# Optimization experiments

Hardware: AMD Instinct MI355X
Metric: run time of the kernel (lower is better)

Reference implementation:

```python
import jax, jax.numpy as jnp
import numpy as np


def setup_inputs() -> dict:
    key = jax.random.key(0)
    ks = jax.random.split(key, 8)
    N, E, F, H = 50000, 400000, 128, 512
    x = jax.random.normal(ks[0], (N, F), dtype=jnp.float32)
    edge_index = jax.random.randint(ks[1], (2, E), 0, N, dtype=jnp.int32)
    W1 = jax.random.normal(ks[2], (H, 2 * F), dtype=jnp.float32) * 0.05
    b1 = jax.random.normal(ks[3], (H,), dtype=jnp.float32) * 0.05
    W2 = jax.random.normal(ks[4], (H, 2 * H), dtype=jnp.float32) * 0.05
    b2 = jax.random.normal(ks[5], (H,), dtype=jnp.float32) * 0.05
    Wo = jax.random.normal(ks[6], (1, H), dtype=jnp.float32) * 0.05
    bo = jax.random.normal(ks[7], (1,), dtype=jnp.float32) * 0.05
    return {"x": x, "edge_index": edge_index, "W1": W1, "b1": b1,
            "W2": W2, "b2": b2, "Wo": Wo, "bo": bo}


def reference(x, edge_index, W1, b1, W2, b2, Wo, bo):
    # GraphSAGE mean aggregation: agg[dst] = mean over incoming edges of h[src]
    N = x.shape[0]
    src = edge_index[0]
    dst = edge_index[1]
    deg = jax.ops.segment_sum(jnp.ones_like(dst, dtype=x.dtype), dst,
                              num_segments=N)
    inv_deg = 1.0 / jnp.maximum(deg, 1.0)  # clamp_min(1.0)

    def agg_mean(h):
        s = jax.ops.segment_sum(h[src], dst, num_segments=N)  # [N, D]
        return s * inv_deg[:, None]

    # Layer 1: concat(self, neigh) -> Linear -> ReLU (dropout = identity, eval)
    n1 = agg_mean(x)
    h1 = jax.nn.relu(jnp.concatenate([x, n1], axis=1) @ W1.T + b1)
    # Layer 2
    n2 = agg_mean(h1)
    h2 = jax.nn.relu(jnp.concatenate([h1, n2], axis=1) @ W2.T + b2)
    # Output head
    logits = h2 @ Wo.T + bo  # [N, 1]
    return jax.nn.sigmoid(logits)
```

## Files before the change

### kernel.cpp

```cpp
#include <hip/hip_runtime.h>
#include <math.h>


typedef __attribute__((ext_vector_type(8))) short bf16x8;
typedef __attribute__((ext_vector_type(4))) float f32x4;

static inline int ceil_div(int a, int b) { return (a + b - 1) / b; }

__device__ inline float bf2f_lo(unsigned u) { return __builtin_bit_cast(float, u << 16); }
__device__ inline float bf2f_hi(unsigned u) { return __builtin_bit_cast(float, u & 0xffff0000u); }
__device__ inline unsigned f2bf(float f) {
    unsigned u = __builtin_bit_cast(unsigned, f);
    u += 0x7fffu + ((u >> 16) & 1u);
    return u >> 16;
}

#define GLOAD_LDS16(gp, lp)                                                   \
    __builtin_amdgcn_global_load_lds(                                         \
        (__attribute__((address_space(1))) void*)(gp),                        \
        (__attribute__((address_space(3))) void*)(lp), 16, 0, 0)


__global__ void cvt3_hist_kernel(const float* __restrict__ a, unsigned short* __restrict__ ao, int na4,
                                 const float* __restrict__ b, unsigned short* __restrict__ bo, int nb4,
                                 const float* __restrict__ c, unsigned short* __restrict__ co, int nc4,
                                 const int* __restrict__ dst, int* __restrict__ deg, int E,
                                 int cvt_blocks) {
    if ((int)blockIdx.x < cvt_blocks) {
        int i = blockIdx.x * 256 + threadIdx.x;
        const float* in; unsigned short* out; int k;
        if (i < na4)                  { in = a; out = ao; k = i; }
        else if (i < na4 + nb4)       { in = b; out = bo; k = i - na4; }
        else if (i < na4 + nb4 + nc4) { in = c; out = co; k = i - na4 - nb4; }
        else return;
        float4 v = ((const float4*)in)[k];
        ushort4 o;
        o.x = (unsigned short)f2bf(v.x);
        o.y = (unsigned short)f2bf(v.y);
        o.z = (unsigned short)f2bf(v.z);
        o.w = (unsigned short)f2bf(v.w);
        ((ushort4*)out)[k] = o;
    } else {
        int e = (blockIdx.x - cvt_blocks) * 256 + threadIdx.x;
        if (e < E) atomicAdd(&deg[dst[e]], 1);
    }
}


__global__ __launch_bounds__(256) void chunk_reduce(const int* __restrict__ deg,
                                                    int* __restrict__ partial, int N) {
    int base = blockIdx.x * 1024;
    int s = 0;
    for (int i = threadIdx.x; i < 1024; i += 256) {
        int idx = base + i;
        if (idx < N) s += deg[idx];
    }
    #pragma unroll
    for (int off = 32; off; off >>= 1) s += __shfl_down(s, off);
    __shared__ int ws[4];
    if ((threadIdx.x & 63) == 0) ws[threadIdx.x >> 6] = s;
    __syncthreads();
    if (threadIdx.x == 0) partial[blockIdx.x] = ws[0] + ws[1] + ws[2] + ws[3];
}

__global__ void partial_scan(int* __restrict__ partial, int* __restrict__ rowstartN, int P) {
    int lane = threadIdx.x;
    int v = (lane < P) ? partial[lane] : 0;
    int incl = v;
    #pragma unroll
    for (int off = 1; off < 64; off <<= 1) {
        int t = __shfl_up(incl, off);
        if (lane >= off) incl += t;
    }
    if (lane < P) partial[lane] = incl - v;
    if (lane == 63) *rowstartN = incl;
}

__global__ __launch_bounds__(256) void chunk_scan(const int* __restrict__ deg,
                                                  const int* __restrict__ partial,
                                                  int* __restrict__ rowstart,
                                                  int* __restrict__ cursor, int N) {
    int base = blockIdx.x * 1024 + threadIdx.x * 4;
    int v[4];
    #pragma unroll
    for (int j = 0; j < 4; ++j) {
        int i = base + j;
        v[j] = (i < N) ? deg[i] : 0;
    }
    int mysum = v[0] + v[1] + v[2] + v[3];
    int incl = mysum;
    int lane = threadIdx.x & 63, wave = threadIdx.x >> 6;
    #pragma unroll
    for (int off = 1; off < 64; off <<= 1) {
        int t = __shfl_up(incl, off);
        if (lane >= off) incl += t;
    }
    __shared__ int ws[4];
    if (lane == 63) ws[wave] = incl;
    __syncthreads();
    int run = partial[blockIdx.x] + incl - mysum;
    for (int w = 0; w < wave; ++w) run += ws[w];
    #pragma unroll
    for (int j = 0; j < 4; ++j) {
        int i = base + j;
        if (i < N) { rowstart[i] = run; cursor[i] = run; }
        run += v[j];
    }
}

__global__ void bucket_kernel(const int* __restrict__ src, const int* __restrict__ dst,
                              int* __restrict__ cursor, int* __restrict__ ebuf, int E) {
    int e = blockIdx.x * 256 + threadIdx.x;
    if (e < E) {
        int pos = atomicAdd(&cursor[dst[e]], 1);
        ebuf[pos] = src[e];
    }
}


__global__ void gather_mean_128(const int* __restrict__ rowstart, const int* __restrict__ ebuf,
                                const unsigned* __restrict__ featb, unsigned* __restrict__ outb, int N) {
    int w = (blockIdx.x * blockDim.x + threadIdx.x) >> 6;
    int lane = threadIdx.x & 63;
    if (w >= N) return;
    int e0 = rowstart[w], e1 = rowstart[w + 1];
    float ax = 0.0f, ay = 0.0f;
    int i = e0;
    for (; i + 8 <= e1; i += 8) {
        unsigned v0 = featb[(size_t)ebuf[i]     * 64 + lane];
        unsigned v1 = featb[(size_t)ebuf[i + 1] * 64 + lane];
        unsigned v2 = featb[(size_t)ebuf[i + 2] * 64 + lane];
        unsigned v3 = featb[(size_t)ebuf[i + 3] * 64 + lane];
        unsigned v4 = featb[(size_t)ebuf[i + 4] * 64 + lane];
        unsigned v5 = featb[(size_t)ebuf[i + 5] * 64 + lane];
        unsigned v6 = featb[(size_t)ebuf[i + 6] * 64 + lane];
        unsigned v7 = featb[(size_t)ebuf[i + 7] * 64 + lane];
        ax += bf2f_lo(v0) + bf2f_lo(v1) + bf2f_lo(v2) + bf2f_lo(v3)
            + bf2f_lo(v4) + bf2f_lo(v5) + bf2f_lo(v6) + bf2f_lo(v7);
        ay += bf2f_hi(v0) + bf2f_hi(v1) + bf2f_hi(v2) + bf2f_hi(v3)
            + bf2f_hi(v4) + bf2f_hi(v5) + bf2f_hi(v6) + bf2f_hi(v7);
    }
    for (; i < e1; ++i) {
        unsigned v = featb[(size_t)ebuf[i] * 64 + lane];
        ax += bf2f_lo(v); ay += bf2f_hi(v);
    }
    float inv = 1.0f / fmaxf((float)(e1 - e0), 1.0f);
    outb[(size_t)w * 64 + lane] = f2bf(ax * inv) | (f2bf(ay * inv) << 16);
}

__global__ void gather_mean_512(const int* __restrict__ rowstart, const int* __restrict__ ebuf,
                                const unsigned short* __restrict__ featb,
                                unsigned short* __restrict__ outb, int N) {
    int w = (blockIdx.x * blockDim.x + threadIdx.x) >> 6;
    int lane = threadIdx.x & 63;
    if (w >= N) return;
    int e0 = rowstart[w], e1 = rowstart[w + 1];
    float a[8] = {0, 0, 0, 0, 0, 0, 0, 0};
    const uint4* base = (const uint4*)featb;
    int i = e0;
    for (; i + 8 <= e1; i += 8) {
        uint4 v0 = base[(size_t)ebuf[i]     * 64 + lane];
        uint4 v1 = base[(size_t)ebuf[i + 1] * 64 + lane];
        uint4 v2 = base[(size_t)ebuf[i + 2] * 64 + lane];
        uint4 v3 = base[(size_t)ebuf[i + 3] * 64 + lane];
        uint4 v4 = base[(size_t)ebuf[i + 4] * 64 + lane];
        uint4 v5 = base[(size_t)ebuf[i + 5] * 64 + lane];
        uint4 v6 = base[(size_t)ebuf[i + 6] * 64 + lane];
        uint4 v7 = base[(size_t)ebuf[i + 7] * 64 + lane];
        a[0] += bf2f_lo(v0.x) + bf2f_lo(v1.x) + bf2f_lo(v2.x) + bf2f_lo(v3.x)
              + bf2f_lo(v4.x) + bf2f_lo(v5.x) + bf2f_lo(v6.x) + bf2f_lo(v7.x);
        a[1] += bf2f_hi(v0.x) + bf2f_hi(v1.x) + bf2f_hi(v2.x) + bf2f_hi(v3.x)
              + bf2f_hi(v4.x) + bf2f_hi(v5.x) + bf2f_hi(v6.x) + bf2f_hi(v7.x);
        a[2] += bf2f_lo(v0.y) + bf2f_lo(v1.y) + bf2f_lo(v2.y) + bf2f_lo(v3.y)
              + bf2f_lo(v4.y) + bf2f_lo(v5.y) + bf2f_lo(v6.y) + bf2f_lo(v7.y);
        a[3] += bf2f_hi(v0.y) + bf2f_hi(v1.y) + bf2f_hi(v2.y) + bf2f_hi(v3.y)
              + bf2f_hi(v4.y) + bf2f_hi(v5.y) + bf2f_hi(v6.y) + bf2f_hi(v7.y);
        a[4] += bf2f_lo(v0.z) + bf2f_lo(v1.z) + bf2f_lo(v2.z) + bf2f_lo(v3.z)
              + bf2f_lo(v4.z) + bf2f_lo(v5.z) + bf2f_lo(v6.z) + bf2f_lo(v7.z);
        a[5] += bf2f_hi(v0.z) + bf2f_hi(v1.z) + bf2f_hi(v2.z) + bf2f_hi(v3.z)
              + bf2f_hi(v4.z) + bf2f_hi(v5.z) + bf2f_hi(v6.z) + bf2f_hi(v7.z);
        a[6] += bf2f_lo(v0.w) + bf2f_lo(v1.w) + bf2f_lo(v2.w) + bf2f_lo(v3.w)
              + bf2f_lo(v4.w) + bf2f_lo(v5.w) + bf2f_lo(v6.w) + bf2f_lo(v7.w);
        a[7] += bf2f_hi(v0.w) + bf2f_hi(v1.w) + bf2f_hi(v2.w) + bf2f_hi(v3.w)
              + bf2f_hi(v4.w) + bf2f_hi(v5.w) + bf2f_hi(v6.w) + bf2f_hi(v7.w);
    }
    for (; i < e1; ++i) {
        uint4 v = base[(size_t)ebuf[i] * 64 + lane];
        a[0] += bf2f_lo(v.x); a[1] += bf2f_hi(v.x);
        a[2] += bf2f_lo(v.y); a[3] += bf2f_hi(v.y);
        a[4] += bf2f_lo(v.z); a[5] += bf2f_hi(v.z);
        a[6] += bf2f_lo(v.w); a[7] += bf2f_hi(v.w);
    }
    float inv = 1.0f / fmaxf((float)(e1 - e0), 1.0f);
    uint4 o;
    o.x = f2bf(a[0] * inv) | (f2bf(a[1] * inv) << 16);
    o.y = f2bf(a[2] * inv) | (f2bf(a[3] * inv) << 16);
    o.z = f2bf(a[4] * inv) | (f2bf(a[5] * inv) << 16);
    o.w = f2bf(a[6] * inv) | (f2bf(a[7] * inv) << 16);
    ((uint4*)outb)[(size_t)w * 64 + lane] = o;
}

__global__ __launch_bounds__(256) void gemm_mfma(
    const unsigned short* __restrict__ A0,
    const unsigned short* __restrict__ A1,
    const unsigned short* __restrict__ W,
    const float* __restrict__ b,
    unsigned short* __restrict__ outb,
    const float* __restrict__ Wo,
    float* __restrict__ logit,
    int N, int K0, int K1, int C, int mode)
{
    const int nrow = (N + 127) >> 7;
    const int id   = blockIdx.x;
    const int rowb = ((id >> 5) << 3) + (id & 7);
    const int colb = (id >> 3) & 3;
    if (rowb >= nrow) return;

    const int K = K0 + K1;
    const int S = K0;
    __shared__ short As[2][4096];
    __shared__ short Bs[2][4096];

    const int tid  = threadIdx.x;
    const int lane = tid & 63;
    const int wave = tid >> 6;
    const int wm = wave & 1, wn = wave >> 1;
    const int cl = lane & 15, quad = lane >> 4;
    const int row0 = rowb * 128;
    const int col0 = colb * 128;

    const int r = lane >> 2;
    const int j = lane & 3;
    const int trow0 = wave * 32 + r;
    const int trow1 = trow0 + 16;
    const int ar0 = (row0 + trow0 < N) ? row0 + trow0 : N - 1;
    const int ar1 = (row0 + trow1 < N) ? row0 + trow1 : N - 1;
    const size_t aoff0 = (size_t)ar0 * S + j * 8;
    const size_t aoff1 = (size_t)ar1 * S + j * 8;
    const size_t boff0 = (size_t)(col0 + trow0) * K + j * 8;
    const size_t boff1 = (size_t)(col0 + trow1) * K + j * 8;
    const int lds0 = (wave * 32) * 32;
    const int lds1 = (wave * 32 + 16) * 32;

    f32x4 acc[4][4];
    #pragma unroll
    for (int mt = 0; mt < 4; ++mt)
        #pragma unroll
        for (int nt = 0; nt < 4; ++nt)
            acc[mt][nt] = (f32x4){0.f, 0.f, 0.f, 0.f};

    GLOAD_LDS16(A0 + aoff0, &As[0][lds0]);
    GLOAD_LDS16(A0 + aoff1, &As[0][lds1]);
    GLOAD_LDS16(W  + boff0, &Bs[0][lds0]);
    GLOAD_LDS16(W  + boff1, &Bs[0][lds1]);

    const int iters = K >> 5;
    for (int i = 0; i < iters; ++i) {
        const int cur = i & 1;
        __syncthreads();
        if (i + 1 < iters) {
            const int kn = (i + 1) << 5;
            const unsigned short* Ab = (kn < K0) ? (A0 + kn) : (A1 + (kn - K0));
            const unsigned short* Wb = W + kn;
            const int nb = cur ^ 1;
            GLOAD_LDS16(Ab + aoff0, &As[nb][lds0]);
            GLOAD_LDS16(Ab + aoff1, &As[nb][lds1]);
            GLOAD_LDS16(Wb + boff0, &Bs[nb][lds0]);
            GLOAD_LDS16(Wb + boff1, &Bs[nb][lds1]);
        }

        bf16x8 af[4], bfr[4];
        #pragma unroll
        for (int mt = 0; mt < 4; ++mt)
            af[mt] = *(const bf16x8*)&As[cur][(wm * 64 + mt * 16 + cl) * 32 + quad * 8];
        #pragma unroll
        for (int nt = 0; nt < 4; ++nt)
            bfr[nt] = *(const bf16x8*)&Bs[cur][(wn * 64 + nt * 16 + cl) * 32 + quad * 8];

        #pragma unroll
        for (int mt = 0; mt < 4; ++mt)
            #pragma unroll
            for (int nt = 0; nt < 4; ++nt)
                acc[mt][nt] = __builtin_amdgcn_mfma_f32_16x16x32_bf16(
                    af[mt], bfr[nt], acc[mt][nt], 0, 0, 0);
    }

    if (mode == 0) {
        #pragma unroll
        for (int nt = 0; nt < 4; ++nt) {
            const int colx = col0 + wn * 64 + nt * 16 + cl;
            const float bb = b[colx];
            #pragma unroll
            for (int mt = 0; mt < 4; ++mt) {
                #pragma unroll
                for (int rr = 0; rr < 4; ++rr) {
                    int row = row0 + wm * 64 + mt * 16 + quad * 4 + rr;
                    if (row < N)
                        outb[(size_t)row * C + colx] =
                            (unsigned short)f2bf(fmaxf(acc[mt][nt][rr] + bb, 0.0f));
                }
            }
        }
    } else {
        float bv[4], wv2[4];
        #pragma unroll
        for (int nt = 0; nt < 4; ++nt) {
            const int colx = col0 + wn * 64 + nt * 16 + cl;
            bv[nt] = b[colx];
            wv2[nt] = Wo[colx];
        }
        #pragma unroll
        for (int mt = 0; mt < 4; ++mt) {
            #pragma unroll
            for (int rr = 0; rr < 4; ++rr) {
                float s = 0.0f;
                #pragma unroll
                for (int nt = 0; nt < 4; ++nt)
                    s += fmaxf(acc[mt][nt][rr] + bv[nt], 0.0f) * wv2[nt];
                s += __shfl_xor(s, 1);
                s += __shfl_xor(s, 2);
                s += __shfl_xor(s, 4);
                s += __shfl_xor(s, 8);
                int row = row0 + wm * 64 + mt * 16 + quad * 4 + rr;
                if (cl == 0 && row < N) atomicAdd(&logit[row], s);
            }
        }
    }
}


#define KT3 32

#define STG3(kt) do {                                                          \
    const unsigned short* _p = ((kt) < 16) ? (A0 + ((kt) << 5))                \
                                           : (A1 + (((kt) - 16) << 5));        \
    const int _bf = (kt) % 3;                                                  \
    GLOAD_LDS16(_p + offA, lds + _bf * 8192 + w * 1024);                       \
    GLOAD_LDS16(W + ((kt) << 5) + offB0,                                       \
                lds + 24576 + _bf * 16384 + w * 2048);                         \
    GLOAD_LDS16(W + ((kt) << 5) + offB1,                                       \
                lds + 24576 + _bf * 16384 + w * 2048 + 1024);                  \
} while (0)

#define RD3(bf) do {                                                           \
    _Pragma("unroll")                                                          \
    for (int _m = 0; _m < 4; ++_m)                                             \
        af[_m] = *(const bf16x8*)(lds + (bf) * 8192 + aoff + _m * 1024);       \
    _Pragma("unroll")                                                          \
    for (int _n = 0; _n < 4; ++_n)                                             \
        bq[_n] = *(const bf16x8*)(lds + 24576 + (bf) * 16384 + boff + _n * 1024); \
} while (0)

#define MM16() do {                                                            \
    _Pragma("unroll")                                                          \
    for (int _m = 0; _m < 4; ++_m)                                             \
        _Pragma("unroll")                                                      \
        for (int _n = 0; _n < 4; ++_n)                                         \
            acc[_m][_n] = __builtin_amdgcn_mfma_f32_16x16x32_bf16(             \
                af[_m], bq[_n], acc[_m][_n], 0, 0, 0);                         \
} while (0)

#define PHASE3(t, stage, gatestr) do {                                         \
    __builtin_amdgcn_sched_barrier(0);                                         \
    asm volatile("s_waitcnt " gatestr ::: "memory");                           \
    __builtin_amdgcn_s_barrier();                                              \
    __builtin_amdgcn_sched_barrier(0);                                         \
    RD3((t) % 3);                                                              \
    if (stage) STG3((t) + 2);                                                  \
    __builtin_amdgcn_s_setprio(1);                                             \
    MM16();                                                                    \
    __builtin_amdgcn_s_setprio(0);                                             \
} while (0)

__global__ __launch_bounds__(512, 4) void gemm2_3buf(
    const unsigned short* __restrict__ A0,
    const unsigned short* __restrict__ A1,
    const unsigned short* __restrict__ W,
    const float* __restrict__ b,
    const float* __restrict__ Wo,
    float* __restrict__ logit,
    int N)
{
    __shared__ char lds[73728];

    const int nwg  = ((N + 127) >> 7) * 2;
    const int orig = blockIdx.x;
    const int xcd = orig & 7, lnum = orig >> 3;
    const int q = nwg >> 3, r = nwg & 7;
    const int virt = (xcd < r ? xcd * (q + 1) : r * (q + 1) + (xcd - r) * q) + lnum;
    const int row0 = (virt >> 1) << 7;
    const int col0 = (virt & 1) << 8;

    const int tid = threadIdx.x;
    const int w = tid >> 6, l = tid & 63;
    const int wr = w >> 2, wc = w & 3;
    const int cl = l & 15, quad = l >> 4;

    const int c_log = (((l & 3) ^ ((l >> 3) & 3))) * 8;
    int ra = row0 + w * 16 + (l >> 2);
    if (ra > N - 1) ra = N - 1;
    const size_t offA  = (size_t)ra * 512 + c_log;
    const size_t offB0 = (size_t)(col0 + w * 32 + (l >> 2)) * 1024 + c_log;
    const size_t offB1 = (size_t)(col0 + w * 32 + 16 + (l >> 2)) * 1024 + c_log;

    const int swz  = ((cl >> 1) & 3) << 4;
    const int aoff = (((wr * 64 + cl) * 64) + quad * 16) ^ swz;
    const int boff = (((wc * 64 + cl) * 64) + quad * 16) ^ swz;

    f32x4 acc[4][4];
    #pragma unroll
    for (int mt = 0; mt < 4; ++mt)
        #pragma unroll
        for (int nt = 0; nt < 4; ++nt)
            acc[mt][nt] = (f32x4){0.f, 0.f, 0.f, 0.f};

    bf16x8 af[4], bq[4];

    STG3(0); STG3(1);

    #pragma unroll
    for (int t = 0; t < 30; ++t)
        PHASE3(t, 1, "vmcnt(3)");
    PHASE3(30, 0, "vmcnt(3)");
    PHASE3(31, 0, "vmcnt(0)");

    float bv[4], wv[4];
    #pragma unroll
    for (int nt = 0; nt < 4; ++nt) {
        const int colx = col0 + wc * 64 + nt * 16 + cl;
        bv[nt] = b[colx];
        wv[nt] = Wo[colx];
    }
    #pragma unroll
    for (int mt = 0; mt < 4; ++mt) {
        #pragma unroll
        for (int rr = 0; rr < 4; ++rr) {
            float s = 0.0f;
            #pragma unroll
            for (int nt = 0; nt < 4; ++nt)
                s += fmaxf(acc[mt][nt][rr] + bv[nt], 0.0f) * wv[nt];
            s += __shfl_xor(s, 1);
            s += __shfl_xor(s, 2);
            s += __shfl_xor(s, 4);
            s += __shfl_xor(s, 8);
            const int row = row0 + wr * 64 + mt * 16 + quad * 4 + rr;
            if (cl == 0 && row < N) atomicAdd(&logit[row], s);
        }
    }
}

__global__ void head_kernel(const float* __restrict__ logit, const float* __restrict__ bo,
                            float* __restrict__ out, int N) {
    int i = blockIdx.x * 256 + threadIdx.x;
    if (i < N) out[i] = 1.0f / (1.0f + expf(-(logit[i] + bo[0])));
}

extern "C" void kernel_launch(void* const* d_in, const int* in_sizes, int n_in,
                              void* d_out, int out_size, void* d_ws, size_t ws_size,
                              hipStream_t stream) {
    const float* x  = (const float*)d_in[0];
    const int*   ei = (const int*)d_in[1];
    const float* W1 = (const float*)d_in[2];
    const float* b1 = (const float*)d_in[3];
    const float* W2 = (const float*)d_in[4];
    const float* b2 = (const float*)d_in[5];
    const float* Wo = (const float*)d_in[6];
    const float* bo = (const float*)d_in[7];
    float* out = (float*)d_out;

    const int N = in_sizes[0] / 128;
    const int E = in_sizes[1] / 2;
    const int* src = ei;
    const int* dst = ei + E;

    char* ws = (char*)d_ws;
    size_t off = 0;
    auto alloc = [&](size_t bytes) {
        void* p = ws + off;
        off += (bytes + 255) & ~(size_t)255;
        return p;
    };
    int* deg      = (int*)alloc((size_t)N * 4);
    int* rowstart = (int*)alloc((size_t)(N + 1) * 4);
    int* cursor   = (int*)alloc((size_t)N * 4);
    int* partial  = (int*)alloc((size_t)64 * 4);
    int* ebuf     = (int*)alloc((size_t)E * 4);
    float* logit  = (float*)alloc((size_t)N * 4);
    unsigned short* xb  = (unsigned short*)alloc((size_t)N * 128 * 2);
    unsigned short* W1b = (unsigned short*)alloc((size_t)512 * 256 * 2);
    unsigned short* W2b = (unsigned short*)alloc((size_t)512 * 1024 * 2);
    unsigned short* n1b = (unsigned short*)alloc((size_t)N * 128 * 2);
    unsigned short* h1b = (unsigned short*)alloc((size_t)N * 512 * 2);
    unsigned short* n2b = (unsigned short*)alloc((size_t)N * 512 * 2);
    (void)ws_size; (void)n_in; (void)out_size;

    hipMemsetAsync(deg,   0, (size_t)N * 4, stream);
    hipMemsetAsync(logit, 0, (size_t)N * 4, stream);

    const int na4 = N * 128 / 4, nb4 = 512 * 256 / 4, nc4 = 512 * 1024 / 4;
    const int cvt_blocks  = ceil_div(na4 + nb4 + nc4, 256);
    const int hist_blocks = ceil_div(E, 256);
    cvt3_hist_kernel<<<cvt_blocks + hist_blocks, 256, 0, stream>>>(
        x, xb, na4, W1, W1b, nb4, W2, W2b, nc4, dst, deg, E, cvt_blocks);

    const int P = ceil_div(N, 1024);
    chunk_reduce<<<P, 256, 0, stream>>>(deg, partial, N);
    partial_scan<<<1, 64, 0, stream>>>(partial, rowstart + N, P);
    chunk_scan<<<P, 256, 0, stream>>>(deg, partial, rowstart, cursor, N);
    bucket_kernel<<<ceil_div(E, 256), 256, 0, stream>>>(src, dst, cursor, ebuf, E);

    const int nrow = ceil_div(N, 128);
    const int gblocks = ceil_div(nrow, 8) * 8 * 4;
    gather_mean_128<<<ceil_div(N * 64, 256), 256, 0, stream>>>(rowstart, ebuf,
                                                               (const unsigned*)xb, (unsigned*)n1b, N);
    gemm_mfma<<<gblocks, 256, 0, stream>>>(xb, n1b, W1b, b1, h1b, nullptr, nullptr,
                                           N, 128, 128, 512, 0);

    gather_mean_512<<<ceil_div(N * 64, 256), 256, 0, stream>>>(rowstart, ebuf, h1b, n2b, N);
    const int g2 = ceil_div(N, 128) * 2;
    gemm2_3buf<<<g2, 512, 0, stream>>>(h1b, n2b, W2b, b2, Wo, logit, N);

    head_kernel<<<ceil_div(N, 256), 256, 0, stream>>>(logit, bo, out, N);
}
```

Before: 335.5 us.

## Pre-swizzle W2 into MFMA fragment layout and stream B operands from global into registers

The conversion kernel now writes W2 in bf16 directly in a per-wave MFMA fragment order. This lets the layer-2 GEMM load each B fragment with one contiguous 16-byte global load per lane straight into registers, prefetched one k-step ahead. Only the A tile is still staged through LDS, so shared memory drops from 72KB to 24KB, which removes B staging and LDS read traffic and may allow more resident workgroups. In exchange, the B loads rely on L1/L2 hits, are duplicated across the two row-waves, and their global latency is hidden by only one phase of lookahead.

```diff
diff --git a/kernel.cpp b/kernel.cpp
--- a/kernel.cpp
+++ b/kernel.cpp
@@ -28,18 +28,35 @@
                                  int cvt_blocks) {
     if ((int)blockIdx.x < cvt_blocks) {
         int i = blockIdx.x * 256 + threadIdx.x;
-        const float* in; unsigned short* out; int k;
-        if (i < na4)                  { in = a; out = ao; k = i; }
-        else if (i < na4 + nb4)       { in = b; out = bo; k = i - na4; }
-        else if (i < na4 + nb4 + nc4) { in = c; out = co; k = i - na4 - nb4; }
-        else return;
-        float4 v = ((const float4*)in)[k];
-        ushort4 o;
-        o.x = (unsigned short)f2bf(v.x);
-        o.y = (unsigned short)f2bf(v.y);
-        o.z = (unsigned short)f2bf(v.z);
-        o.w = (unsigned short)f2bf(v.w);
-        ((ushort4*)out)[k] = o;
+        if (i < na4 + nb4) {
+            const float* in; unsigned short* out; int k;
+            if (i < na4) { in = a; out = ao; k = i; }
+            else         { in = b; out = bo; k = i - na4; }
+            float4 v = ((const float4*)in)[k];
+            ushort4 o;
+            o.x = (unsigned short)f2bf(v.x);
+            o.y = (unsigned short)f2bf(v.y);
+            o.z = (unsigned short)f2bf(v.z);
+            o.w = (unsigned short)f2bf(v.w);
+            ((ushort4*)out)[k] = o;
+        } else if (i < na4 + nb4 + nc4) {
+            int kk = i - na4 - nb4;
+            float4 v = ((const float4*)c)[kk];
+            ushort4 o;
+            o.x = (unsigned short)f2bf(v.x);
+            o.y = (unsigned short)f2bf(v.y);
+            o.z = (unsigned short)f2bf(v.z);
+            o.w = (unsigned short)f2bf(v.w);
+            const int cc = kk >> 8;
+            const int kq = kk & 255;
+            const int t    = kq >> 3;
+            const int quad = (kq >> 1) & 3;
+            const int j0   = (kq & 1) * 4;
+            const int g  = cc >> 6, nt = (cc >> 4) & 3, cl = cc & 15;
+            const size_t off =
+                ((((size_t)(t * 8 + g) * 4 + nt) * 4 + quad) * 16 + cl) * 8 + j0;
+            *(ushort4*)(co + off) = o;
+        }
     } else {
         int e = (blockIdx.x - cvt_blocks) * 256 + threadIdx.x;
         if (e < E) atomicAdd(&deg[dst[e]], 1);
@@ -329,29 +346,26 @@
 }
 
 
-#define KT3 32
-
-#define STG3(kt) do {                                                          \
+#define STGA(kt) do {                                                          \
     const unsigned short* _p = ((kt) < 16) ? (A0 + ((kt) << 5))                \
                                            : (A1 + (((kt) - 16) << 5));        \
-    const int _bf = (kt) % 3;                                                  \
-    GLOAD_LDS16(_p + offA, lds + _bf * 8192 + w * 1024);                       \
-    GLOAD_LDS16(W + ((kt) << 5) + offB0,                                       \
-                lds + 24576 + _bf * 16384 + w * 2048);                         \
-    GLOAD_LDS16(W + ((kt) << 5) + offB1,                                       \
-                lds + 24576 + _bf * 16384 + w * 2048 + 1024);                  \
+    GLOAD_LDS16(_p + offA, lds + ((kt) % 3) * 8192 + w * 1024);                \
 } while (0)
 
-#define RD3(bf) do {                                                           \
+#define LDB(kt) do {                                                           \
+    _Pragma("unroll")                                                          \
+    for (int _n = 0; _n < 4; ++_n)                                             \
+        bq[_n] = *(const bf16x8*)(W +                                          \
+            (((size_t)(kt) * 8 + gB) * 4 + _n) * 512 + l * 8);                 \
+} while (0)
+
+#define RDA(bf) do {                                                           \
     _Pragma("unroll")                                                          \
     for (int _m = 0; _m < 4; ++_m)                                             \
         af[_m] = *(const bf16x8*)(lds + (bf) * 8192 + aoff + _m * 1024);       \
-    _Pragma("unroll")                                                          \
-    for (int _n = 0; _n < 4; ++_n)                                             \
-        bq[_n] = *(const bf16x8*)(lds + 24576 + (bf) * 16384 + boff + _n * 1024); \
 } while (0)
 
-#define MM16() do {                                                            \
+#define MM16B() do {                                                           \
     _Pragma("unroll")                                                          \
     for (int _m = 0; _m < 4; ++_m)                                             \
         _Pragma("unroll")                                                      \
@@ -360,19 +374,20 @@
                 af[_m], bq[_n], acc[_m][_n], 0, 0, 0);                         \
 } while (0)
 
-#define PHASE3(t, stage, gatestr) do {                                         \
+#define PHASE4(t, stage) do {                                                  \
     __builtin_amdgcn_sched_barrier(0);                                         \
-    asm volatile("s_waitcnt " gatestr ::: "memory");                           \
+    asm volatile("s_waitcnt vmcnt(5)" ::: "memory");                           \
     __builtin_amdgcn_s_barrier();                                              \
     __builtin_amdgcn_sched_barrier(0);                                         \
-    RD3((t) % 3);                                                              \
-    if (stage) STG3((t) + 2);                                                  \
+    RDA((t) % 3);                                                              \
+    if (stage) STGA((t) + 2);                                                  \
     __builtin_amdgcn_s_setprio(1);                                             \
-    MM16();                                                                    \
+    MM16B();                                                                   \
     __builtin_amdgcn_s_setprio(0);                                             \
+    if ((t) + 1 < 32) LDB((t) + 1);                                            \
 } while (0)
 
-__global__ __launch_bounds__(512, 4) void gemm2_3buf(
+__global__ __launch_bounds__(512, 4) void gemm2_breg(
     const unsigned short* __restrict__ A0,
     const unsigned short* __restrict__ A1,
     const unsigned short* __restrict__ W,
@@ -381,7 +396,7 @@
     float* __restrict__ logit,
     int N)
 {
-    __shared__ char lds[73728];
+    __shared__ char lds[24576];
 
     const int nwg  = ((N + 127) >> 7) * 2;
     const int orig = blockIdx.x;
@@ -395,17 +410,15 @@
     const int w = tid >> 6, l = tid & 63;
     const int wr = w >> 2, wc = w & 3;
     const int cl = l & 15, quad = l >> 4;
+    const int gB = (col0 >> 6) + wc;
 
     const int c_log = (((l & 3) ^ ((l >> 3) & 3))) * 8;
     int ra = row0 + w * 16 + (l >> 2);
     if (ra > N - 1) ra = N - 1;
-    const size_t offA  = (size_t)ra * 512 + c_log;
-    const size_t offB0 = (size_t)(col0 + w * 32 + (l >> 2)) * 1024 + c_log;
-    const size_t offB1 = (size_t)(col0 + w * 32 + 16 + (l >> 2)) * 1024 + c_log;
+    const size_t offA = (size_t)ra * 512 + c_log;
 
     const int swz  = ((cl >> 1) & 3) << 4;
     const int aoff = (((wr * 64 + cl) * 64) + quad * 16) ^ swz;
-    const int boff = (((wc * 64 + cl) * 64) + quad * 16) ^ swz;
 
     f32x4 acc[4][4];
     #pragma unroll
@@ -416,13 +429,15 @@
 
     bf16x8 af[4], bq[4];
 
-    STG3(0); STG3(1);
+    STGA(0); STGA(1);
+    LDB(0);
 
     #pragma unroll
     for (int t = 0; t < 30; ++t)
-        PHASE3(t, 1, "vmcnt(3)");
-    PHASE3(30, 0, "vmcnt(3)");
-    PHASE3(31, 0, "vmcnt(0)");
+        PHASE4(t, 1);
+    PHASE4(30, 0);
+    PHASE4(31, 0);
+    asm volatile("s_waitcnt vmcnt(0)" ::: "memory");
 
     float bv[4], wv[4];
     #pragma unroll
@@ -518,7 +533,7 @@
 
     gather_mean_512<<<ceil_div(N * 64, 256), 256, 0, stream>>>(rowstart, ebuf, h1b, n2b, N);
     const int g2 = ceil_div(N, 128) * 2;
-    gemm2_3buf<<<g2, 512, 0, stream>>>(h1b, n2b, W2b, b2, Wo, logit, N);
+    gemm2_breg<<<g2, 512, 0, stream>>>(h1b, n2b, W2b, b2, Wo, logit, N);
 
     head_kernel<<<ceil_div(N, 256), 256, 0, stream>>>(logit, bo, out, N);
 }
```

Result: no change. 330.6 us (-1.5%).
